# Performance work log

Hardware: AMD Instinct MI355X
Metric: run time of the kernel (lower is better)

## Reference

```python
import jax, jax.numpy as jnp
import numpy as np

VOCAB = 1000
EMB = 64
HID = 64


def _lstm_last(x, mask, Wx, Wh, b):
    """Keras-style LSTM over time, returning final hidden state.

    x:    [T, B, EMB] float
    mask: [T, B] bool  (False = padded step: state carried through, Keras mask_zero semantics)
    Wx:   [EMB, 4H], Wh: [H, 4H], b: [4H]; gate order i, f, g(c), o.
    """
    T, B, _ = x.shape
    h0 = jnp.zeros((B, HID), x.dtype)
    c0 = jnp.zeros((B, HID), x.dtype)

    def step(carry, inp):
        h, c = carry
        x_t, m_t = inp
        z = x_t @ Wx + h @ Wh + b                      # [B, 4H]
        i, f, g, o = jnp.split(z, 4, axis=-1)
        i = jax.nn.sigmoid(i)
        f = jax.nn.sigmoid(f)
        o = jax.nn.sigmoid(o)
        c_new = f * c + i * jnp.tanh(g)
        h_new = o * jnp.tanh(c_new)
        m = m_t[:, None]
        h = jnp.where(m, h_new, h)
        c = jnp.where(m, c_new, c)
        return (h, c), None

    (h_T, _), _ = jax.lax.scan(step, (h0, c0), (x, mask))
    return h_T


def setup_inputs() -> dict:
    key = jax.random.key(0)
    ks = jax.random.split(key, 8)
    B, T = 512, 1024
    tokens = jax.random.randint(ks[0], (B, T), 0, VOCAB, dtype=jnp.int32)
    emb_table = jax.random.normal(ks[1], (VOCAB, EMB), jnp.float32) * 0.05
    def glorot(k, shape):
        lim = np.sqrt(6.0 / (shape[0] + shape[1]))
        return jax.random.uniform(k, shape, jnp.float32, -lim, lim)
    # Keras unit_forget_bias: bias of forget gate initialized to 1.
    b_init = jnp.concatenate([jnp.zeros(HID), jnp.ones(HID), jnp.zeros(2 * HID)]).astype(jnp.float32)
    return {
        "tokens": tokens,
        "emb_table": emb_table,
        "Wx_f": glorot(ks[2], (EMB, 4 * HID)),
        "Wh_f": glorot(ks[3], (HID, 4 * HID)),
        "b_f": b_init,
        "Wx_b": glorot(ks[4], (EMB, 4 * HID)),
        "Wh_b": glorot(ks[5], (HID, 4 * HID)),
        "b_b": b_init,
    }


def reference(tokens, emb_table, Wx_f, Wh_f, b_f, Wx_b, Wh_b, b_b):
    # Embedding with mask_zero=True: token 0 is masked.
    emb = emb_table[tokens]                  # [B, T, EMB]
    mask = tokens != 0                       # [B, T]
    x = jnp.transpose(emb, (1, 0, 2))        # [T, B, EMB]
    m = jnp.transpose(mask, (1, 0))          # [T, B]
    h_fwd = _lstm_last(x, m, Wx_f, Wh_f, b_f)
    # Backward direction: Keras go_backwards reverses the sequence (and mask).
    h_bwd = _lstm_last(x[::-1], m[::-1], Wx_b, Wh_b, b_b)
    return jnp.concatenate([h_fwd, h_bwd], axis=-1)  # [B, 2H]
```

## Files before the change

kernel.cpp:

```cpp
#include <hip/hip_runtime.h>

#define T_STEPS 1024
#define B_TOT   512
#define VOCAB   1000
#define EMB     64
#define HID     64
#define GATES   256

typedef float f4 __attribute__((ext_vector_type(4)));
typedef float f2 __attribute__((ext_vector_type(2)));

__device__ __forceinline__ float fast_rcp(float x)  { return __builtin_amdgcn_rcpf(x); }
__device__ __forceinline__ float fast_exp2(float x) { return __builtin_amdgcn_exp2f(x); }

__device__ __forceinline__ float sigmoid_f(float x) {
    return fast_rcp(1.0f + fast_exp2(-1.4426950408889634f * x));
}
__device__ __forceinline__ float tanh_f(float x) {
    float e = fast_exp2(2.8853900817779268f * x);
    return 1.0f - 2.0f * fast_rcp(e + 1.0f);
}

__global__ __launch_bounds__(256, 4)
void zx_table_kernel(const float* __restrict__ emb,
                     const float* __restrict__ Wx_f, const float* __restrict__ b_f,
                     const float* __restrict__ Wx_b, const float* __restrict__ b_b,
                     float* __restrict__ zx_tab)
{
    const int bid = blockIdx.x;
    const int dir = bid / VOCAB;
    const int v   = bid - dir * VOCAB;
    const int j   = threadIdx.x;
    const int p   = j & 1;
    const int u   = (j >> 1) & 63;
    const int w   = j >> 7;
    const int col = (2 * w + p) * HID + u;

    const float* __restrict__ Wx = dir ? Wx_b : Wx_f;
    const float* __restrict__ bv = dir ? b_b  : b_f;

    __shared__ float4 x4[EMB / 4];
    if (j < EMB / 4) x4[j] = ((const float4*)emb)[v * (EMB / 4) + j];
    __syncthreads();

    float a0 = bv[col], a1 = 0.f, a2 = 0.f, a3 = 0.f;
#pragma unroll
    for (int q = 0; q < EMB / 4; ++q) {
        float4 xv = x4[q];
        a0 = fmaf(xv.x, Wx[(4 * q + 0) * GATES + col], a0);
        a1 = fmaf(xv.y, Wx[(4 * q + 1) * GATES + col], a1);
        a2 = fmaf(xv.z, Wx[(4 * q + 2) * GATES + col], a2);
        a3 = fmaf(xv.w, Wx[(4 * q + 3) * GATES + col], a3);
    }
    zx_tab[(dir * VOCAB + v) * GATES + j] = (a0 + a1) + (a2 + a3);
}

__global__ __launch_bounds__(128, 2)
void lstm_rec_kernel(const int* __restrict__ tokens,
                     const float* __restrict__ Wh_f,
                     const float* __restrict__ Wh_b,
                     const float* __restrict__ zx_tab,
                     float* __restrict__ out)
{
    const int bx  = blockIdx.x;
    const int dir = bx >> 9;
    const int row = bx & 511;
    const int u   = threadIdx.x & 63;
    const int w   = threadIdx.x >> 6;

    const float* __restrict__ Wh   = dir ? Wh_b : Wh_f;
    const f2*    __restrict__ zx2  = (const f2*)(zx_tab + dir * (VOCAB * GATES));
    const int*   __restrict__ trow = tokens + row * T_STEPS;

    const int colA = (2 * w) * HID + u;
    const int colB = colA + HID;
    float whA[HID], whB[HID];
#pragma unroll
    for (int k = 0; k < HID; ++k) whA[k] = Wh[k * GATES + colA];
#pragma unroll
    for (int k = 0; k < HID; ++k) whB[k] = Wh[k * GATES + colB];

    __shared__ float hbuf[HID];
    __shared__ f2    act2[HID];

    if (threadIdx.x < HID) hbuf[threadIdx.x] = 0.0f;
    float c = 0.0f;
    __syncthreads();

    int tokc = trow[dir ? (T_STEPS - 1) : 0];
    int tokn = trow[dir ? (T_STEPS - 2) : 1];
    f2  zxc  = zx2[tokc * 128 + w * 64 + u];

    const f4* __restrict__ hb4 = (const f4*)hbuf;

#pragma unroll 1
    for (int t = 0; t < T_STEPS; ++t) {
        int t2   = (t + 2 < T_STEPS) ? (t + 2) : (T_STEPS - 1);
        int tokf = trow[dir ? (T_STEPS - 1 - t2) : t2];
        f2  zxn  = zx2[tokn * 128 + w * 64 + u];

        float aA0 = zxc.x, aA1 = 0.f, aA2 = 0.f, aA3 = 0.f;
        float aB0 = zxc.y, aB1 = 0.f, aB2 = 0.f, aB3 = 0.f;
#pragma unroll
        for (int q = 0; q < HID / 4; ++q) {
            f4 hv = hb4[q];
            aA0 = fmaf(hv.x, whA[4 * q + 0], aA0);
            aA1 = fmaf(hv.y, whA[4 * q + 1], aA1);
            aA2 = fmaf(hv.z, whA[4 * q + 2], aA2);
            aA3 = fmaf(hv.w, whA[4 * q + 3], aA3);
            aB0 = fmaf(hv.x, whB[4 * q + 0], aB0);
            aB1 = fmaf(hv.y, whB[4 * q + 1], aB1);
            aB2 = fmaf(hv.z, whB[4 * q + 2], aB2);
            aB3 = fmaf(hv.w, whB[4 * q + 3], aB3);
        }
        float zA = (aA0 + aA1) + (aA2 + aA3);
        float zB = (aB0 + aB1) + (aB2 + aB3);

        float actA, actB;
        if (w == 0) {
            actA = sigmoid_f(zA);
            actB = sigmoid_f(zB);
        } else {
            actA = tanh_f(zA);
            actB = sigmoid_f(zB);
            f2 go; go.x = actA; go.y = actB;
            act2[u] = go;
        }
        __syncthreads();

        if (w == 0 && tokc != 0) {
            f2 go = act2[u];
            c = fmaf(actB, c, actA * go.x);
            hbuf[u] = go.y * tanh_f(c);
        }
        __syncthreads();

        tokc = tokn; tokn = tokf; zxc = zxn;
    }

    if (w == 0)
        out[row * (2 * HID) + dir * HID + u] = hbuf[u];
}

extern "C" void kernel_launch(void* const* d_in, const int* in_sizes, int n_in,
                              void* d_out, int out_size, void* d_ws, size_t ws_size,
                              hipStream_t stream) {
    const int*   tokens = (const int*)  d_in[0];
    const float* emb    = (const float*)d_in[1];
    const float* Wx_f   = (const float*)d_in[2];
    const float* Wh_f   = (const float*)d_in[3];
    const float* b_f    = (const float*)d_in[4];
    const float* Wx_b   = (const float*)d_in[5];
    const float* Wh_b   = (const float*)d_in[6];
    const float* b_b    = (const float*)d_in[7];
    float* out = (float*)d_out;

    float* zx_tab = (float*)d_ws;

    hipLaunchKernelGGL(zx_table_kernel, dim3(2 * VOCAB), dim3(GATES), 0, stream,
                       emb, Wx_f, b_f, Wx_b, b_b, zx_tab);
    hipLaunchKernelGGL(lstm_rec_kernel, dim3(2 * B_TOT), dim3(128), 0, stream,
                       tokens, Wh_f, Wh_b, zx_tab, out);
}
```

Measured before the change: 626.2 us.

## Halve per-step barriers with double-buffered gate exchange and redundant cell update

Each recurrent step now uses a single block barrier instead of two. Both waves swap their activated gates through double-buffered shared arrays, and each wave computes the cell and hidden update on its own, writing identical hbuf values. The whole step, including the matvec, is skipped for masked tokens. This removes one barrier and the idle wave-1 phase per step, at the cost of duplicated tanh/FMA work and extra shared memory. The occupancy hint also moves from min-blocks to an explicit waves-per-EU attribute.

```diff
diff --git a/kernel.cpp b/kernel.cpp
--- a/kernel.cpp
+++ b/kernel.cpp
@@ -55,7 +55,7 @@
     zx_tab[(dir * VOCAB + v) * GATES + j] = (a0 + a1) + (a2 + a3);
 }
 
-__global__ __launch_bounds__(128, 2)
+__global__ __launch_bounds__(128) __attribute__((amdgpu_waves_per_eu(2, 2)))
 void lstm_rec_kernel(const int* __restrict__ tokens,
                      const float* __restrict__ Wh_f,
                      const float* __restrict__ Wh_b,
@@ -81,10 +81,13 @@
     for (int k = 0; k < HID; ++k) whB[k] = Wh[k * GATES + colB];
 
     __shared__ float hbuf[HID];
-    __shared__ f2    act2[HID];
+    __shared__ float sA[2][2][HID];
+    __shared__ float sB[2][2][HID];
 
     if (threadIdx.x < HID) hbuf[threadIdx.x] = 0.0f;
-    float c = 0.0f;
+    float c    = 0.0f;
+    float hval = 0.0f;
+    int   p    = 0;
     __syncthreads();
 
     int tokc = trow[dir ? (T_STEPS - 1) : 0];
@@ -99,47 +102,47 @@
         int tokf = trow[dir ? (T_STEPS - 1 - t2) : t2];
         f2  zxn  = zx2[tokn * 128 + w * 64 + u];
 
-        float aA0 = zxc.x, aA1 = 0.f, aA2 = 0.f, aA3 = 0.f;
-        float aB0 = zxc.y, aB1 = 0.f, aB2 = 0.f, aB3 = 0.f;
+        if (tokc != 0) {
+            float aA0 = zxc.x, aA1 = 0.f, aA2 = 0.f, aA3 = 0.f;
+            float aB0 = zxc.y, aB1 = 0.f, aB2 = 0.f, aB3 = 0.f;
 #pragma unroll
-        for (int q = 0; q < HID / 4; ++q) {
-            f4 hv = hb4[q];
-            aA0 = fmaf(hv.x, whA[4 * q + 0], aA0);
-            aA1 = fmaf(hv.y, whA[4 * q + 1], aA1);
-            aA2 = fmaf(hv.z, whA[4 * q + 2], aA2);
-            aA3 = fmaf(hv.w, whA[4 * q + 3], aA3);
-            aB0 = fmaf(hv.x, whB[4 * q + 0], aB0);
-            aB1 = fmaf(hv.y, whB[4 * q + 1], aB1);
-            aB2 = fmaf(hv.z, whB[4 * q + 2], aB2);
-            aB3 = fmaf(hv.w, whB[4 * q + 3], aB3);
+            for (int q = 0; q < HID / 4; ++q) {
+                f4 hv = hb4[q];
+                aA0 = fmaf(hv.x, whA[4 * q + 0], aA0);
+                aA1 = fmaf(hv.y, whA[4 * q + 1], aA1);
+                aA2 = fmaf(hv.z, whA[4 * q + 2], aA2);
+                aA3 = fmaf(hv.w, whA[4 * q + 3], aA3);
+                aB0 = fmaf(hv.x, whB[4 * q + 0], aB0);
+                aB1 = fmaf(hv.y, whB[4 * q + 1], aB1);
+                aB2 = fmaf(hv.z, whB[4 * q + 2], aB2);
+                aB3 = fmaf(hv.w, whB[4 * q + 3], aB3);
+            }
+            float zA = (aA0 + aA1) + (aA2 + aA3);
+            float zB = (aB0 + aB1) + (aB2 + aB3);
+
+            float actA = w ? tanh_f(zA) : sigmoid_f(zA);
+            float actB = sigmoid_f(zB);
+            sA[p][w][u] = actA;
+            sB[p][w][u] = actB;
+            __syncthreads();
+
+            float oA = sA[p][w ^ 1][u];
+            float oB = sB[p][w ^ 1][u];
+            float ig = w ? oA   : actA;
+            float fg = w ? oB   : actB;
+            float gg = w ? actA : oA;
+            float og = w ? actB : oB;
+            c    = fmaf(fg, c, ig * gg);
+            hval = og * tanh_f(c);
+            hbuf[u] = hval;
+            p ^= 1;
         }
-        float zA = (aA0 + aA1) + (aA2 + aA3);
-        float zB = (aB0 + aB1) + (aB2 + aB3);
-
-        float actA, actB;
-        if (w == 0) {
-            actA = sigmoid_f(zA);
-            actB = sigmoid_f(zB);
-        } else {
-            actA = tanh_f(zA);
-            actB = sigmoid_f(zB);
-            f2 go; go.x = actA; go.y = actB;
-            act2[u] = go;
-        }
-        __syncthreads();
-
-        if (w == 0 && tokc != 0) {
-            f2 go = act2[u];
-            c = fmaf(actB, c, actA * go.x);
-            hbuf[u] = go.y * tanh_f(c);
-        }
-        __syncthreads();
 
         tokc = tokn; tokn = tokf; zxc = zxn;
     }
 
     if (w == 0)
-        out[row * (2 * HID) + dir * HID + u] = hbuf[u];
+        out[row * (2 * HID) + dir * HID + u] = hval;
 }
 
 extern "C" void kernel_launch(void* const* d_in, const int* in_sizes, int n_in,
```

Result: slower. 715.2 us (+14.2%).

## Process two batch rows per LSTM block to reuse register-resident Wh

Applied to the files above, without the earlier changes.

Each recurrent block now handles two batch rows of the same direction. The Wh columns already held in registers are reused for both rows, and the grid is halved to 512 blocks. This doubles the independent FMA work per barrier, so each step's latency and synchronisation cost is spread over two sequences. The risk is higher register pressure, since there are now more accumulators alongside 128 weight registers, and fewer blocks to fill the CUs.

```diff
diff --git a/kernel.cpp b/kernel.cpp
--- a/kernel.cpp
+++ b/kernel.cpp
@@ -62,84 +62,117 @@
                      const float* __restrict__ zx_tab,
                      float* __restrict__ out)
 {
-    const int bx  = blockIdx.x;
-    const int dir = bx >> 9;
-    const int row = bx & 511;
-    const int u   = threadIdx.x & 63;
-    const int w   = threadIdx.x >> 6;
+    const int bx   = blockIdx.x;
+    const int dir  = bx >> 8;
+    const int rp   = bx & 255;
+    const int rowA = rp * 2, rowB = rp * 2 + 1;
+    const int u    = threadIdx.x & 63;
+    const int w    = threadIdx.x >> 6;
 
-    const float* __restrict__ Wh   = dir ? Wh_b : Wh_f;
-    const f2*    __restrict__ zx2  = (const f2*)(zx_tab + dir * (VOCAB * GATES));
-    const int*   __restrict__ trow = tokens + row * T_STEPS;
+    const float* __restrict__ Wh    = dir ? Wh_b : Wh_f;
+    const f2*    __restrict__ zx2   = (const f2*)(zx_tab + dir * (VOCAB * GATES));
+    const int*   __restrict__ trowA = tokens + rowA * T_STEPS;
+    const int*   __restrict__ trowB = tokens + rowB * T_STEPS;
 
-    const int colA = (2 * w) * HID + u;
-    const int colB = colA + HID;
-    float whA[HID], whB[HID];
+    const int colE = (2 * w) * HID + u;
+    const int colO = colE + HID;
+    float whE[HID], whO[HID];
 #pragma unroll
-    for (int k = 0; k < HID; ++k) whA[k] = Wh[k * GATES + colA];
+    for (int k = 0; k < HID; ++k) whE[k] = Wh[k * GATES + colE];
 #pragma unroll
-    for (int k = 0; k < HID; ++k) whB[k] = Wh[k * GATES + colB];
+    for (int k = 0; k < HID; ++k) whO[k] = Wh[k * GATES + colO];
 
-    __shared__ float hbuf[HID];
-    __shared__ f2    act2[HID];
+    __shared__ float hbA[HID], hbB[HID];
+    __shared__ f2    acA[HID], acB[HID];
 
-    if (threadIdx.x < HID) hbuf[threadIdx.x] = 0.0f;
-    float c = 0.0f;
+    if (threadIdx.x < HID) hbA[threadIdx.x] = 0.0f;
+    else                   hbB[threadIdx.x - HID] = 0.0f;
+    float cA = 0.0f, cB = 0.0f;
     __syncthreads();
 
-    int tokc = trow[dir ? (T_STEPS - 1) : 0];
-    int tokn = trow[dir ? (T_STEPS - 2) : 1];
-    f2  zxc  = zx2[tokc * 128 + w * 64 + u];
+    int tA0 = trowA[dir ? (T_STEPS - 1) : 0];
+    int tA1 = trowA[dir ? (T_STEPS - 2) : 1];
+    int tB0 = trowB[dir ? (T_STEPS - 1) : 0];
+    int tB1 = trowB[dir ? (T_STEPS - 2) : 1];
+    f2 zxAc = zx2[tA0 * 128 + w * 64 + u];
+    f2 zxBc = zx2[tB0 * 128 + w * 64 + u];
 
-    const f4* __restrict__ hb4 = (const f4*)hbuf;
+    const f4* __restrict__ hb4A = (const f4*)hbA;
+    const f4* __restrict__ hb4B = (const f4*)hbB;
 
 #pragma unroll 1
     for (int t = 0; t < T_STEPS; ++t) {
-        int t2   = (t + 2 < T_STEPS) ? (t + 2) : (T_STEPS - 1);
-        int tokf = trow[dir ? (T_STEPS - 1 - t2) : t2];
-        f2  zxn  = zx2[tokn * 128 + w * 64 + u];
+        int t2  = (t + 2 < T_STEPS) ? (t + 2) : (T_STEPS - 1);
+        int sp  = dir ? (T_STEPS - 1 - t2) : t2;
+        int tA2 = trowA[sp];
+        int tB2 = trowB[sp];
+        f2 zxAn = zx2[tA1 * 128 + w * 64 + u];
+        f2 zxBn = zx2[tB1 * 128 + w * 64 + u];
 
-        float aA0 = zxc.x, aA1 = 0.f, aA2 = 0.f, aA3 = 0.f;
-        float aB0 = zxc.y, aB1 = 0.f, aB2 = 0.f, aB3 = 0.f;
+        float eA0 = zxAc.x, eA1 = 0.f, eA2 = 0.f, eA3 = 0.f;
+        float oA0 = zxAc.y, oA1 = 0.f, oA2 = 0.f, oA3 = 0.f;
+        float eB0 = zxBc.x, eB1 = 0.f, eB2 = 0.f, eB3 = 0.f;
+        float oB0 = zxBc.y, oB1 = 0.f, oB2 = 0.f, oB3 = 0.f;
 #pragma unroll
         for (int q = 0; q < HID / 4; ++q) {
-            f4 hv = hb4[q];
-            aA0 = fmaf(hv.x, whA[4 * q + 0], aA0);
-            aA1 = fmaf(hv.y, whA[4 * q + 1], aA1);
-            aA2 = fmaf(hv.z, whA[4 * q + 2], aA2);
-            aA3 = fmaf(hv.w, whA[4 * q + 3], aA3);
-            aB0 = fmaf(hv.x, whB[4 * q + 0], aB0);
-            aB1 = fmaf(hv.y, whB[4 * q + 1], aB1);
-            aB2 = fmaf(hv.z, whB[4 * q + 2], aB2);
-            aB3 = fmaf(hv.w, whB[4 * q + 3], aB3);
+            f4 hA = hb4A[q];
+            f4 hB = hb4B[q];
+            eA0 = fmaf(hA.x, whE[4 * q + 0], eA0);
+            eA1 = fmaf(hA.y, whE[4 * q + 1], eA1);
+            eA2 = fmaf(hA.z, whE[4 * q + 2], eA2);
+            eA3 = fmaf(hA.w, whE[4 * q + 3], eA3);
+            oA0 = fmaf(hA.x, whO[4 * q + 0], oA0);
+            oA1 = fmaf(hA.y, whO[4 * q + 1], oA1);
+            oA2 = fmaf(hA.z, whO[4 * q + 2], oA2);
+            oA3 = fmaf(hA.w, whO[4 * q + 3], oA3);
+            eB0 = fmaf(hB.x, whE[4 * q + 0], eB0);
+            eB1 = fmaf(hB.y, whE[4 * q + 1], eB1);
+            eB2 = fmaf(hB.z, whE[4 * q + 2], eB2);
+            eB3 = fmaf(hB.w, whE[4 * q + 3], eB3);
+            oB0 = fmaf(hB.x, whO[4 * q + 0], oB0);
+            oB1 = fmaf(hB.y, whO[4 * q + 1], oB1);
+            oB2 = fmaf(hB.z, whO[4 * q + 2], oB2);
+            oB3 = fmaf(hB.w, whO[4 * q + 3], oB3);
         }
-        float zA = (aA0 + aA1) + (aA2 + aA3);
-        float zB = (aB0 + aB1) + (aB2 + aB3);
+        float zEA = (eA0 + eA1) + (eA2 + eA3);
+        float zOA = (oA0 + oA1) + (oA2 + oA3);
+        float zEB = (eB0 + eB1) + (eB2 + eB3);
+        float zOB = (oB0 + oB1) + (oB2 + oB3);
 
-        float actA, actB;
+        float aEA, aOA, aEB, aOB;
         if (w == 0) {
-            actA = sigmoid_f(zA);
-            actB = sigmoid_f(zB);
+            aEA = sigmoid_f(zEA); aOA = sigmoid_f(zOA);
+            aEB = sigmoid_f(zEB); aOB = sigmoid_f(zOB);
         } else {
-            actA = tanh_f(zA);
-            actB = sigmoid_f(zB);
-            f2 go; go.x = actA; go.y = actB;
-            act2[u] = go;
+            aEA = tanh_f(zEA);    aOA = sigmoid_f(zOA);
+            aEB = tanh_f(zEB);    aOB = sigmoid_f(zOB);
+            f2 gA; gA.x = aEA; gA.y = aOA; acA[u] = gA;
+            f2 gB; gB.x = aEB; gB.y = aOB; acB[u] = gB;
         }
         __syncthreads();
 
-        if (w == 0 && tokc != 0) {
-            f2 go = act2[u];
-            c = fmaf(actB, c, actA * go.x);
-            hbuf[u] = go.y * tanh_f(c);
+        if (w == 0) {
+            f2 goA = acA[u];
+            f2 goB = acB[u];
+            if (tA0 != 0) {
+                cA = fmaf(aOA, cA, aEA * goA.x);
+                hbA[u] = goA.y * tanh_f(cA);
+            }
+            if (tB0 != 0) {
+                cB = fmaf(aOB, cB, aEB * goB.x);
+                hbB[u] = goB.y * tanh_f(cB);
+            }
         }
         __syncthreads();
 
-        tokc = tokn; tokn = tokf; zxc = zxn;
+        tA0 = tA1; tA1 = tA2; zxAc = zxAn;
+        tB0 = tB1; tB1 = tB2; zxBc = zxBn;
     }
 
-    if (w == 0)
-        out[row * (2 * HID) + dir * HID + u] = hbuf[u];
+    if (w == 0) {
+        out[rowA * (2 * HID) + dir * HID + u] = hbA[u];
+        out[rowB * (2 * HID) + dir * HID + u] = hbB[u];
+    }
 }
 
 extern "C" void kernel_launch(void* const* d_in, const int* in_sizes, int n_in,
@@ -159,6 +192,6 @@
 
     hipLaunchKernelGGL(zx_table_kernel, dim3(2 * VOCAB), dim3(GATES), 0, stream,
                        emb, Wx_f, b_f, Wx_b, b_b, zx_tab);
-    hipLaunchKernelGGL(lstm_rec_kernel, dim3(2 * B_TOT), dim3(128), 0, stream,
+    hipLaunchKernelGGL(lstm_rec_kernel, dim3(B_TOT), dim3(128), 0, stream,
                        tokens, Wh_f, Wh_b, zx_tab, out);
 }
```

Measured after the change: 1.089 ms. +73.8%, slower.

## Interleave two batch rows per block to overlap cell updates with gate matvecs

Applied to the files above, without the earlier changes.

Each recurrent block now handles two batch rows, with the grid halved to 512 blocks. The two rows are processed in a staggered schedule: while one wave finishes row A's cell/hidden update, the other computes row B's, so the serial update phase of one row overlaps the matvec of the other. This is meant to hide the idle half-block during the cell-update phase and the barrier latency, sharing the register-resident Wh across two rows. The cost is fewer blocks (less parallelism across CUs) and twice the serial work per block, plus more complex state handoff through shared memory.

```diff
diff --git a/kernel.cpp b/kernel.cpp
--- a/kernel.cpp
+++ b/kernel.cpp
@@ -62,84 +62,146 @@
                      const float* __restrict__ zx_tab,
                      float* __restrict__ out)
 {
-    const int bx  = blockIdx.x;
-    const int dir = bx >> 9;
-    const int row = bx & 511;
-    const int u   = threadIdx.x & 63;
-    const int w   = threadIdx.x >> 6;
-
-    const float* __restrict__ Wh   = dir ? Wh_b : Wh_f;
-    const f2*    __restrict__ zx2  = (const f2*)(zx_tab + dir * (VOCAB * GATES));
-    const int*   __restrict__ trow = tokens + row * T_STEPS;
-
-    const int colA = (2 * w) * HID + u;
-    const int colB = colA + HID;
-    float whA[HID], whB[HID];
-#pragma unroll
-    for (int k = 0; k < HID; ++k) whA[k] = Wh[k * GATES + colA];
-#pragma unroll
-    for (int k = 0; k < HID; ++k) whB[k] = Wh[k * GATES + colB];
-
-    __shared__ float hbuf[HID];
-    __shared__ f2    act2[HID];
-
-    if (threadIdx.x < HID) hbuf[threadIdx.x] = 0.0f;
-    float c = 0.0f;
+    const int bx   = blockIdx.x;
+    const int dir  = bx >> 8;
+    const int rp   = bx & 255;
+    const int rowA = rp * 2, rowB = rp * 2 + 1;
+    const int u    = threadIdx.x & 63;
+    const int w    = threadIdx.x >> 6;
+
+    const float* __restrict__ Wh  = dir ? Wh_b : Wh_f;
+    const f2*    __restrict__ zx2 = (const f2*)(zx_tab + dir * (VOCAB * GATES));
+    const int*   __restrict__ trA = tokens + rowA * T_STEPS;
+    const int*   __restrict__ trB = tokens + rowB * T_STEPS;
+
+    const int colE = (2 * w) * HID + u;
+    const int colO = colE + HID;
+    float whE[HID], whO[HID];
+#pragma unroll
+    for (int k = 0; k < HID; ++k) whE[k] = Wh[k * GATES + colE];
+#pragma unroll
+    for (int k = 0; k < HID; ++k) whO[k] = Wh[k * GATES + colO];
+
+    __shared__ float hA[HID], hB[HID];
+    __shared__ f2 actAgo[HID];
+    __shared__ f2 actBif[HID];
+
+    if (threadIdx.x < HID) hA[threadIdx.x] = 0.0f;
+    else                   hB[threadIdx.x - HID] = 0.0f;
+
+    float cA = 0.f, cB = 0.f;
+    float hAv = 0.f, hBv = 0.f;
+    float aAe = 0.f, aAo = 0.f;
+    float aBe = 0.f, aBo = 0.f;
+
+#define POS(t) (dir ? (T_STEPS - 1 - (t)) : (t))
+    int tAc = trA[POS(0)], tAn = trA[POS(1)];
+    int tBc = trB[POS(0)], tBn = trB[POS(1)];
+    int tBp = 0;
+    f2 zxAc = zx2[tAc * 128 + w * 64 + u];
+    f2 zxBc = zx2[tBc * 128 + w * 64 + u];
+
+    const f4* __restrict__ hA4 = (const f4*)hA;
+    const f4* __restrict__ hB4 = (const f4*)hB;
+
     __syncthreads();
-
-    int tokc = trow[dir ? (T_STEPS - 1) : 0];
-    int tokn = trow[dir ? (T_STEPS - 2) : 1];
-    f2  zxc  = zx2[tokc * 128 + w * 64 + u];
-
-    const f4* __restrict__ hb4 = (const f4*)hbuf;
 
 #pragma unroll 1
     for (int t = 0; t < T_STEPS; ++t) {
-        int t2   = (t + 2 < T_STEPS) ? (t + 2) : (T_STEPS - 1);
-        int tokf = trow[dir ? (T_STEPS - 1 - t2) : t2];
-        f2  zxn  = zx2[tokn * 128 + w * 64 + u];
-
-        float aA0 = zxc.x, aA1 = 0.f, aA2 = 0.f, aA3 = 0.f;
-        float aB0 = zxc.y, aB1 = 0.f, aB2 = 0.f, aB3 = 0.f;
+        const int sp = POS((t + 2 < T_STEPS) ? (t + 2) : (T_STEPS - 1));
+
+        int tAf = trA[sp];
+        f2  zxAn = zx2[tAn * 128 + w * 64 + u];
+
+        float e0 = zxAc.x, e1 = 0.f, e2 = 0.f, e3 = 0.f;
+        float o0 = zxAc.y, o1 = 0.f, o2 = 0.f, o3 = 0.f;
 #pragma unroll
         for (int q = 0; q < HID / 4; ++q) {
-            f4 hv = hb4[q];
-            aA0 = fmaf(hv.x, whA[4 * q + 0], aA0);
-            aA1 = fmaf(hv.y, whA[4 * q + 1], aA1);
-            aA2 = fmaf(hv.z, whA[4 * q + 2], aA2);
-            aA3 = fmaf(hv.w, whA[4 * q + 3], aA3);
-            aB0 = fmaf(hv.x, whB[4 * q + 0], aB0);
-            aB1 = fmaf(hv.y, whB[4 * q + 1], aB1);
-            aB2 = fmaf(hv.z, whB[4 * q + 2], aB2);
-            aB3 = fmaf(hv.w, whB[4 * q + 3], aB3);
-        }
-        float zA = (aA0 + aA1) + (aA2 + aA3);
-        float zB = (aB0 + aB1) + (aB2 + aB3);
-
-        float actA, actB;
+            f4 hv = hA4[q];
+            e0 = fmaf(hv.x, whE[4 * q + 0], e0);
+            e1 = fmaf(hv.y, whE[4 * q + 1], e1);
+            e2 = fmaf(hv.z, whE[4 * q + 2], e2);
+            e3 = fmaf(hv.w, whE[4 * q + 3], e3);
+            o0 = fmaf(hv.x, whO[4 * q + 0], o0);
+            o1 = fmaf(hv.y, whO[4 * q + 1], o1);
+            o2 = fmaf(hv.z, whO[4 * q + 2], o2);
+            o3 = fmaf(hv.w, whO[4 * q + 3], o3);
+        }
+        float zAe = (e0 + e1) + (e2 + e3);
+        float zAo = (o0 + o1) + (o2 + o3);
+
         if (w == 0) {
-            actA = sigmoid_f(zA);
-            actB = sigmoid_f(zB);
+            aAe = sigmoid_f(zAe);
+            aAo = sigmoid_f(zAo);
         } else {
-            actA = tanh_f(zA);
-            actB = sigmoid_f(zB);
-            f2 go; go.x = actA; go.y = actB;
-            act2[u] = go;
+            aAe = tanh_f(zAe);
+            aAo = sigmoid_f(zAo);
+            f2 v; v.x = aAe; v.y = aAo;
+            actAgo[u] = v;
+            if (t > 0) {
+                f2 bif = actBif[u];
+                if (tBp != 0) {
+                    cB  = fmaf(bif.y, cB, bif.x * aBe);
+                    hBv = aBo * tanh_f(cB);
+                }
+                hB[u] = hBv;
+            }
         }
         __syncthreads();
 
-        if (w == 0 && tokc != 0) {
-            f2 go = act2[u];
-            c = fmaf(actB, c, actA * go.x);
-            hbuf[u] = go.y * tanh_f(c);
+        int tBf = trB[sp];
+        f2  zxBn = zx2[tBn * 128 + w * 64 + u];
+
+        e0 = zxBc.x; e1 = 0.f; e2 = 0.f; e3 = 0.f;
+        o0 = zxBc.y; o1 = 0.f; o2 = 0.f; o3 = 0.f;
+#pragma unroll
+        for (int q = 0; q < HID / 4; ++q) {
+            f4 hv = hB4[q];
+            e0 = fmaf(hv.x, whE[4 * q + 0], e0);
+            e1 = fmaf(hv.y, whE[4 * q + 1], e1);
+            e2 = fmaf(hv.z, whE[4 * q + 2], e2);
+            e3 = fmaf(hv.w, whE[4 * q + 3], e3);
+            o0 = fmaf(hv.x, whO[4 * q + 0], o0);
+            o1 = fmaf(hv.y, whO[4 * q + 1], o1);
+            o2 = fmaf(hv.z, whO[4 * q + 2], o2);
+            o3 = fmaf(hv.w, whO[4 * q + 3], o3);
+        }
+        float zBe = (e0 + e1) + (e2 + e3);
+        float zBo = (o0 + o1) + (o2 + o3);
+
+        if (w == 0) {
+            aBe = sigmoid_f(zBe);
+            aBo = sigmoid_f(zBo);
+            f2 v; v.x = aBe; v.y = aBo;
+            actBif[u] = v;
+            f2 ago = actAgo[u];
+            if (tAc != 0) {
+                cA  = fmaf(aAo, cA, aAe * ago.x);
+                hAv = ago.y * tanh_f(cA);
+            }
+            hA[u] = hAv;
+        } else {
+            aBe = tanh_f(zBe);
+            aBo = sigmoid_f(zBo);
         }
         __syncthreads();
 
-        tokc = tokn; tokn = tokf; zxc = zxn;
+        tBp = tBc;
+        tAc = tAn; tAn = tAf; zxAc = zxAn;
+        tBc = tBn; tBn = tBf; zxBc = zxBn;
     }
 
-    if (w == 0)
-        out[row * (2 * HID) + dir * HID + u] = hbuf[u];
+    if (w == 1) {
+        f2 bif = actBif[u];
+        if (tBp != 0) {
+            cB  = fmaf(bif.y, cB, bif.x * aBe);
+            hBv = aBo * tanh_f(cB);
+        }
+        out[rowB * (2 * HID) + dir * HID + u] = hBv;
+    } else {
+        out[rowA * (2 * HID) + dir * HID + u] = hAv;
+    }
+#undef POS
 }
 
 extern "C" void kernel_launch(void* const* d_in, const int* in_sizes, int n_in,
@@ -159,6 +221,6 @@
 
     hipLaunchKernelGGL(zx_table_kernel, dim3(2 * VOCAB), dim3(GATES), 0, stream,
                        emb, Wx_f, b_f, Wx_b, b_b, zx_tab);
-    hipLaunchKernelGGL(lstm_rec_kernel, dim3(2 * B_TOT), dim3(128), 0, stream,
+    hipLaunchKernelGGL(lstm_rec_kernel, dim3(B_TOT), dim3(128), 0, stream,
                        tokens, Wh_f, Wh_b, zx_tab, out);
 }
```

New measurement: 1.169 ms. 1.87x slower.
